# Kernel tuning notes

Measured on AMD Instinct MI355X. Metric: run time of the kernel, lower is better.

The kernel has to match this reference:

```python
import jax, jax.numpy as jnp
import numpy as np

EPS = 1e-5

def setup_inputs() -> dict:
    key = jax.random.key(0)
    ks = jax.random.split(key, 8)
    B, C, H, W = 8, 128, 128, 128
    return {
        "x1": jax.random.normal(ks[0], (B, C, H, W), jnp.float32),
        "x2": jax.random.normal(ks[1], (B, C, H, W), jnp.float32),
        "se_w1": jax.random.normal(ks[2], (C // 4, 2 * C), jnp.float32) * 0.05,
        "se_w2": jax.random.normal(ks[3], (2 * C, C // 4), jnp.float32) * 0.05,
        "conv_w": jax.random.normal(ks[4], (C, 2 * C, 3, 3), jnp.float32) * 0.05,
        "bn_gamma": jnp.ones((C,), jnp.float32),
        "bn_beta": jnp.zeros((C,), jnp.float32),
        "bn_mean": jax.random.normal(ks[5], (C,), jnp.float32) * 0.1,
        "bn_var": jax.random.uniform(ks[6], (C,), jnp.float32, 0.5, 1.5),
        "gamma": jax.random.uniform(ks[7], (1,), jnp.float32),
    }

def reference(x1, x2, se_w1, se_w2, conv_w, bn_gamma, bn_beta, bn_mean, bn_var, gamma):
    B, C, H, W = x1.shape
    x = jnp.concatenate([x1, x2], axis=1)                      # [B,2C,H,W]
    # SE gate: global avg pool -> Linear/ReLU/Linear/Sigmoid
    avg = jnp.mean(x, axis=(2, 3))                             # [B,2C]
    h = jax.nn.relu(avg @ se_w1.T)                             # [B,C//4]
    se = jax.nn.sigmoid(h @ se_w2.T)                           # [B,2C]
    x = x * se[:, :, None, None]
    # ConvBNReLU (3x3, pad 1, eval-mode BN)
    x = jax.lax.conv_general_dilated(
        x, conv_w, window_strides=(1, 1), padding="SAME",
        dimension_numbers=("NCHW", "OIHW", "NCHW"))           # [B,C,H,W]
    inv = bn_gamma / jnp.sqrt(bn_var + EPS)
    x = jax.nn.relu(x * inv[None, :, None, None]
                    + (bn_beta - bn_mean * inv)[None, :, None, None])
    # Channel self-attention with max-subtraction trick
    q = x.reshape(B, C, H * W)                                 # query = key = value
    sim = jnp.einsum("bcn,bdn->bcd", q, q)                     # [B,C,C]
    sim = jnp.max(sim, axis=-1, keepdims=True) - sim
    sim = jax.nn.softmax(sim, axis=-1)
    feat = jnp.einsum("bcd,bdn->bcn", sim, q).reshape(B, C, H, W)
    return gamma * feat + x
```

## Files before the change

kernel.cpp:

```cpp
#include <hip/hip_runtime.h>
#include <math.h>

#define B_   8
#define C_   128
#define C2_  256
#define H_   128
#define W_   128
#define HW_  16384
#define CR_  32
#define EPS_ 1e-5f
#define NS_  32

typedef _Float16 f16;
typedef f16 f16x8 __attribute__((ext_vector_type(8)));
typedef f16 f16x4 __attribute__((ext_vector_type(4)));
typedef float f32x4 __attribute__((ext_vector_type(4)));

__global__ __launch_bounds__(256) void prep_kernel(
    const float* __restrict__ x1, const float* __restrict__ x2,
    float* __restrict__ avg_sums, f16* __restrict__ xs)
{
    __shared__ f16 T[W_ * 136];
    __shared__ float part[C2_];
    int h = blockIdx.x, b = blockIdx.y;
    int tid = threadIdx.x;
    part[tid] = 0.f;
    f16* out = xs + ((size_t)b * H_ + h) * W_ * C2_;
    for (int p = 0; p < 2; ++p) {
        const float* src = p ? x2 : x1;
        __syncthreads();
        for (int idx = tid; idx < C_ * 32; idx += 256) {
            int c = idx >> 5, w4 = (idx & 31) << 2;
            const float4 v = *(const float4*)&src[(((size_t)b * C_ + c) * H_ + h) * W_ + w4];
            float s = v.x + v.y + v.z + v.w;
            s += __shfl_xor(s, 1, 64);  s += __shfl_xor(s, 2, 64);
            s += __shfl_xor(s, 4, 64);  s += __shfl_xor(s, 8, 64);
            s += __shfl_xor(s, 16, 64);
            if ((tid & 31) == 0) part[p * C_ + c] = s;
            int cs = c ^ (8 * ((idx & 31) & 15));
            T[(w4 + 0) * 136 + cs] = (f16)v.x;
            T[(w4 + 1) * 136 + cs] = (f16)v.y;
            T[(w4 + 2) * 136 + cs] = (f16)v.z;
            T[(w4 + 3) * 136 + cs] = (f16)v.w;
        }
        __syncthreads();
        for (int u = tid; u < W_ * 16; u += 256) {
            int w = u >> 4, o = u & 15;
            f16x8 v = *(const f16x8*)&T[w * 136 + ((o * 8) ^ (8 * ((w >> 2) & 15)))];
            *(f16x8*)&out[w * C2_ + p * C_ + o * 8] = v;
        }
    }
    __syncthreads();
    atomicAdd(&avg_sums[b * C2_ + tid], part[tid]);
}

__global__ __launch_bounds__(256) void se_mlp_kernel(
    const float* __restrict__ avg_sums, const float* __restrict__ w1,
    const float* __restrict__ w2, float* __restrict__ se)
{
    __shared__ float s_avg[B_ * C2_];
    __shared__ float s_h[B_ * CR_];
    for (int i = threadIdx.x; i < B_ * C2_; i += 256)
        s_avg[i] = avg_sums[i] * (1.f / (float)HW_);
    __syncthreads();
    {
        int i = threadIdx.x;
        int b = i / CR_, j = i % CR_;
        float s = 0.f;
        for (int k = 0; k < C2_; ++k) s += s_avg[b * C2_ + k] * w1[j * C2_ + k];
        s_h[i] = fmaxf(s, 0.f);
    }
    __syncthreads();
    for (int i = threadIdx.x; i < B_ * C2_; i += 256) {
        int b = i / C2_, c = i % C2_;
        float s = 0.f;
        #pragma unroll
        for (int j = 0; j < CR_; ++j) s += s_h[b * CR_ + j] * w2[c * CR_ + j];
        se[i] = 1.f / (1.f + expf(-s));
    }
}

__global__ __launch_bounds__(256) void wt_build_kernel(
    const float* __restrict__ conv_w, f16* __restrict__ wt)
{
    int idx = blockIdx.x * 256 + threadIdx.x;
    int ci = idx & 31;
    int co = (idx >> 5) & 127;
    int cc = (idx >> 12) & 7;
    int t  = idx >> 15;
    wt[idx] = (f16)conv_w[((size_t)co * C2_ + cc * 32 + ci) * 9 + t];
}

#define XROW 130
#define XPAD 40

__global__ __launch_bounds__(256, 3) void conv_mfma_kernel(
    const f16* __restrict__ xs, const f16* __restrict__ wt,
    const float* __restrict__ se,
    const float* __restrict__ bn_gamma, const float* __restrict__ bn_beta,
    const float* __restrict__ bn_mean, const float* __restrict__ bn_var,
    f16* __restrict__ yh, f16* __restrict__ yt)
{
    __shared__ f16 Xs[3 * XROW * XPAD];
    __shared__ __align__(16) f16 seh[C2_];
    int h = blockIdx.x, b = blockIdx.y;
    int tid = threadIdx.x;
    int wave = tid >> 6, lane = tid & 63;
    int wm = wave >> 1, wn = wave & 1;
    int lr = lane & 15, kg = lane >> 4;
    const f16* xsb = xs + (size_t)b * ((size_t)H_ * W_ * C2_);

    seh[tid] = (f16)se[b * C2_ + tid];

    f32x4 acc[4][4];
    #pragma unroll
    for (int i = 0; i < 4; ++i)
        #pragma unroll
        for (int j = 0; j < 4; ++j)
            #pragma unroll
            for (int r = 0; r < 4; ++r) acc[i][j][r] = 0.f;

    auto ldaf = [&](int cc, int t, f16x8* dst) {
        const f16* wb = wt + ((size_t)(t * 8 + cc) * C_) * 32;
        #pragma unroll
        for (int i = 0; i < 4; ++i)
            dst[i] = *(const f16x8*)&wb[(wm * 64 + i * 16 + lr) * 32 + kg * 8];
    };

    f16x8 af3[3][4];
    ldaf(0, 0, af3[0]);
    ldaf(0, 1, af3[1]);

    for (int cc = 0; cc < 8; ++cc) {
        __syncthreads();
        for (int u = tid; u < 3 * XROW * 4; u += 256) {
            int r = u / (XROW * 4);
            int rem = u - r * (XROW * 4);
            int col = rem >> 2, q = rem & 3;
            int gh = h + r - 1, gw = col - 1;
            f16x8 v;
            #pragma unroll
            for (int z = 0; z < 8; ++z) v[z] = (f16)0.f;
            if ((unsigned)gh < (unsigned)H_ && (unsigned)gw < (unsigned)W_) {
                v = *(const f16x8*)&xsb[((size_t)(gh * W_ + gw)) * C2_ + cc * 32 + q * 8];
                f16x8 sv = *(const f16x8*)&seh[cc * 32 + q * 8];
                v = v * sv;
            }
            *(f16x8*)&Xs[(r * XROW + col) * XPAD + q * 8] = v;
        }
        __syncthreads();
        #pragma unroll
        for (int t = 0; t < 9; ++t) {
            const int dh = t / 3, dw = t % 3;
            {
                int pt = t + 2, pcc = cc;
                if (pt >= 9) { pt -= 9; ++pcc; }
                if (pcc < 8) ldaf(pcc, pt, af3[(t + 2) % 3]);
            }
            f16x8 bf[4];
            #pragma unroll
            for (int j = 0; j < 4; ++j)
                bf[j] = *(const f16x8*)&Xs[(dh * XROW + (wn * 64 + j * 16 + lr + dw)) * XPAD + kg * 8];
            const f16x8* af = af3[t % 3];
            #pragma unroll
            for (int i = 0; i < 4; ++i)
                #pragma unroll
                for (int j = 0; j < 4; ++j)
                    acc[i][j] = __builtin_amdgcn_mfma_f32_16x16x32_f16(af[i], bf[j], acc[i][j], 0, 0, 0);
        }
    }
    #pragma unroll
    for (int i = 0; i < 4; ++i) {
        int cb = wm * 64 + i * 16 + kg * 4;
        float inv[4], add[4];
        #pragma unroll
        for (int r = 0; r < 4; ++r) {
            int c = cb + r;
            inv[r] = bn_gamma[c] * rsqrtf(bn_var[c] + EPS_);
            add[r] = bn_beta[c] - bn_mean[c] * inv[r];
        }
        #pragma unroll
        for (int j = 0; j < 4; ++j) {
            int n = wn * 64 + j * 16 + lr;
            f16x4 tv;
            #pragma unroll
            for (int r = 0; r < 4; ++r) {
                float v = fmaxf(acc[i][j][r] * inv[r] + add[r], 0.f);
                tv[r] = (f16)v;
                yh[((size_t)b * C_ + cb + r) * HW_ + h * W_ + n] = (f16)v;
            }
            *(f16x4*)&yt[((size_t)b * HW_ + h * W_ + n) * C_ + cb] = tv;
        }
    }
}

__global__ __launch_bounds__(512) void sim_mfma_kernel(
    const f16* __restrict__ yh, float* __restrict__ simp)
{
    int ns = blockIdx.x, b = blockIdx.y;
    int tid = threadIdx.x, wave = tid >> 6, lane = tid & 63;
    int wm = wave >> 2, wn = wave & 3;
    int lr = lane & 15, kg = lane >> 4;
    const f16* Y = yh + (size_t)b * C_ * HW_;
    int n0 = ns * (HW_ / NS_);

    f32x4 acc[4][2];
    #pragma unroll
    for (int i = 0; i < 4; ++i)
        #pragma unroll
        for (int j = 0; j < 2; ++j)
            #pragma unroll
            for (int r = 0; r < 4; ++r) acc[i][j][r] = 0.f;

    for (int kk = 0; kk < 16; ++kk) {
        int k = n0 + kk * 32 + kg * 8;
        f16x8 af[4], bf[2];
        #pragma unroll
        for (int i = 0; i < 4; ++i)
            af[i] = *(const f16x8*)&Y[(size_t)(wm * 64 + i * 16 + lr) * HW_ + k];
        #pragma unroll
        for (int j = 0; j < 2; ++j)
            bf[j] = *(const f16x8*)&Y[(size_t)(wn * 32 + j * 16 + lr) * HW_ + k];
        #pragma unroll
        for (int i = 0; i < 4; ++i)
            #pragma unroll
            for (int j = 0; j < 2; ++j)
                acc[i][j] = __builtin_amdgcn_mfma_f32_16x16x32_f16(af[i], bf[j], acc[i][j], 0, 0, 0);
    }
    float* dst = simp + (size_t)(ns * B_ + b) * C_ * C_;
    #pragma unroll
    for (int i = 0; i < 4; ++i)
        #pragma unroll
        for (int j = 0; j < 2; ++j)
            #pragma unroll
            for (int r = 0; r < 4; ++r)
                dst[(wm * 64 + i * 16 + kg * 4 + r) * C_ + wn * 32 + j * 16 + lr] = acc[i][j][r];
}

__global__ __launch_bounds__(128) void softmax_kernel(
    const float* __restrict__ simp, f16* __restrict__ Ph)
{
    int bc = blockIdx.x;
    int b = bc / C_;
    int d = threadIdx.x;
    float s = 0.f;
    for (int ns = 0; ns < NS_; ++ns)
        s += simp[((size_t)(ns * B_ + b) * C_ + (bc % C_)) * C_ + d];
    float v = -s;
    float m = v;
    #pragma unroll
    for (int off = 32; off > 0; off >>= 1) m = fmaxf(m, __shfl_xor(m, off, 64));
    __shared__ float sm[2], ss[2];
    int wid = threadIdx.x >> 6;
    if ((threadIdx.x & 63) == 0) sm[wid] = m;
    __syncthreads();
    m = fmaxf(sm[0], sm[1]);
    float p = expf(v - m);
    float sum = p;
    #pragma unroll
    for (int off = 32; off > 0; off >>= 1) sum += __shfl_xor(sum, off, 64);
    if ((threadIdx.x & 63) == 0) ss[wid] = sum;
    __syncthreads();
    sum = ss[0] + ss[1];
    Ph[(size_t)bc * C_ + d] = (f16)(p / sum);
}

__global__ __launch_bounds__(256) void feat_mfma_kernel(
    const f16* __restrict__ Ph, const f16* __restrict__ yt,
    const float* __restrict__ gamma, float* __restrict__ out)
{
    int nt = blockIdx.x, b = blockIdx.y;
    int tid = threadIdx.x, wave = tid >> 6, lane = tid & 63;
    int wm = wave >> 1, wn = wave & 1;
    int lr = lane & 15, kg = lane >> 4;
    int n0 = nt * 128;
    const f16* Pb = Ph + (size_t)b * C_ * C_;
    const f16* Yt = yt + (size_t)b * HW_ * C_;

    f32x4 acc[4][4];
    #pragma unroll
    for (int i = 0; i < 4; ++i)
        #pragma unroll
        for (int j = 0; j < 4; ++j)
            #pragma unroll
            for (int r = 0; r < 4; ++r) acc[i][j][r] = 0.f;

    #pragma unroll
    for (int kk = 0; kk < 4; ++kk) {
        int k = kk * 32 + kg * 8;
        f16x8 af[4], bf[4];
        #pragma unroll
        for (int i = 0; i < 4; ++i)
            af[i] = *(const f16x8*)&Pb[(wm * 64 + i * 16 + lr) * C_ + k];
        #pragma unroll
        for (int j = 0; j < 4; ++j)
            bf[j] = *(const f16x8*)&Yt[(size_t)(n0 + wn * 64 + j * 16 + lr) * C_ + k];
        #pragma unroll
        for (int i = 0; i < 4; ++i)
            #pragma unroll
            for (int j = 0; j < 4; ++j)
                acc[i][j] = __builtin_amdgcn_mfma_f32_16x16x32_f16(af[i], bf[j], acc[i][j], 0, 0, 0);
    }
    float g = gamma[0];
    #pragma unroll
    for (int i = 0; i < 4; ++i) {
        int cb = wm * 64 + i * 16 + kg * 4;
        #pragma unroll
        for (int j = 0; j < 4; ++j) {
            int n = n0 + wn * 64 + j * 16 + lr;
            f16x4 rv = *(const f16x4*)&Yt[(size_t)n * C_ + cb];
            #pragma unroll
            for (int r = 0; r < 4; ++r)
                out[((size_t)b * C_ + cb + r) * HW_ + n] = g * acc[i][j][r] + (float)rv[r];
        }
    }
}

extern "C" void kernel_launch(void* const* d_in, const int* in_sizes, int n_in,
                              void* d_out, int out_size, void* d_ws, size_t ws_size,
                              hipStream_t stream)
{
    const float* x1       = (const float*)d_in[0];
    const float* x2       = (const float*)d_in[1];
    const float* se_w1    = (const float*)d_in[2];
    const float* se_w2    = (const float*)d_in[3];
    const float* conv_w   = (const float*)d_in[4];
    const float* bn_gamma = (const float*)d_in[5];
    const float* bn_beta  = (const float*)d_in[6];
    const float* bn_mean  = (const float*)d_in[7];
    const float* bn_var   = (const float*)d_in[8];
    const float* gamma    = (const float*)d_in[9];
    float* out = (float*)d_out;

    char* ws = (char*)d_ws;
    float* avg  = (float*)(ws);
    float* se   = (float*)(ws + 8192);
    f16*   Ph   = (f16*)  (ws + 16384);
    f16*   wt   = (f16*)  (ws + 278528);
    f16*   xs   = (f16*)  (ws + 1048576);
    float* simp = (float*)(ws + 1048576);
    f16*   yh   = (f16*)  (ws + 68157440);
    f16*   yt   = (f16*)  (ws + 101711872);

    hipMemsetAsync(avg, 0, B_ * C2_ * sizeof(float), stream);
    prep_kernel<<<dim3(H_, B_), 256, 0, stream>>>(x1, x2, avg, xs);
    se_mlp_kernel<<<dim3(1), 256, 0, stream>>>(avg, se_w1, se_w2, se);
    wt_build_kernel<<<dim3(1152), 256, 0, stream>>>(conv_w, wt);
    conv_mfma_kernel<<<dim3(H_, B_), 256, 0, stream>>>(
        xs, wt, se, bn_gamma, bn_beta, bn_mean, bn_var, yh, yt);
    sim_mfma_kernel<<<dim3(NS_, B_), 512, 0, stream>>>(yh, simp);
    softmax_kernel<<<dim3(B_ * C_), 128, 0, stream>>>(simp, Ph);
    feat_mfma_kernel<<<dim3(HW_ / 128, B_), 256, 0, stream>>>(Ph, yt, gamma, out);
}
```

Measured before the change: 405.1 us.

## Compute two output rows per conv block and stage yt stores through LDS

The conv kernel now processes two output rows per block, with each wave covering all 128 output channels over 32 columns. Each weight fragment load is therefore reused across both rows, and the halo input tile is shared by four rows instead of three, with a new LDS layout indexed by channel group. The transposed yt output is written through shared memory so that global stores are coalesced 16-byte rows, and the feat kernel now reads the residual from the channel-major yh, so its residual reads match the output layout. In exchange, each thread holds more accumulators, occupancy drops to 2 blocks, the grid is halved, and the weight prefetch now only covers the next tap rather than two taps ahead.

```diff
diff --git a/kernel.cpp b/kernel.cpp
--- a/kernel.cpp
+++ b/kernel.cpp
@@ -91,53 +91,50 @@
     wt[idx] = (f16)conv_w[((size_t)co * C2_ + cc * 32 + ci) * 9 + t];
 }
 
-#define XROW 130
-#define XPAD 40
-
-__global__ __launch_bounds__(256, 3) void conv_mfma_kernel(
+__global__ __launch_bounds__(256, 2) void conv_mfma_kernel(
     const f16* __restrict__ xs, const f16* __restrict__ wt,
     const float* __restrict__ se,
     const float* __restrict__ bn_gamma, const float* __restrict__ bn_beta,
     const float* __restrict__ bn_mean, const float* __restrict__ bn_var,
     f16* __restrict__ yh, f16* __restrict__ yt)
 {
-    __shared__ f16 Xs[3 * XROW * XPAD];
+    __shared__ f16 Xs[17408];
     __shared__ __align__(16) f16 seh[C2_];
-    int h = blockIdx.x, b = blockIdx.y;
+    int h0 = blockIdx.x * 2, b = blockIdx.y;
     int tid = threadIdx.x;
     int wave = tid >> 6, lane = tid & 63;
-    int wm = wave >> 1, wn = wave & 1;
+    int wn = wave;
     int lr = lane & 15, kg = lane >> 4;
     const f16* xsb = xs + (size_t)b * ((size_t)H_ * W_ * C2_);
 
     seh[tid] = (f16)se[b * C2_ + tid];
 
-    f32x4 acc[4][4];
-    #pragma unroll
-    for (int i = 0; i < 4; ++i)
-        #pragma unroll
-        for (int j = 0; j < 4; ++j)
-            #pragma unroll
-            for (int r = 0; r < 4; ++r) acc[i][j][r] = 0.f;
-
+    f32x4 acc[2][8][2];
+    #pragma unroll
+    for (int o = 0; o < 2; ++o)
+        #pragma unroll
+        for (int i = 0; i < 8; ++i)
+            #pragma unroll
+            for (int j = 0; j < 2; ++j)
+                #pragma unroll
+                for (int r = 0; r < 4; ++r) acc[o][i][j][r] = 0.f;
+
+    f16x8 afb[2][8];
     auto ldaf = [&](int cc, int t, f16x8* dst) {
         const f16* wb = wt + ((size_t)(t * 8 + cc) * C_) * 32;
         #pragma unroll
-        for (int i = 0; i < 4; ++i)
-            dst[i] = *(const f16x8*)&wb[(wm * 64 + i * 16 + lr) * 32 + kg * 8];
+        for (int i = 0; i < 8; ++i)
+            dst[i] = *(const f16x8*)&wb[(i * 16 + lr) * 32 + kg * 8];
     };
 
-    f16x8 af3[3][4];
-    ldaf(0, 0, af3[0]);
-    ldaf(0, 1, af3[1]);
-
     for (int cc = 0; cc < 8; ++cc) {
         __syncthreads();
-        for (int u = tid; u < 3 * XROW * 4; u += 256) {
-            int r = u / (XROW * 4);
-            int rem = u - r * (XROW * 4);
+        ldaf(cc, 0, afb[0]);
+        for (int u = tid; u < 4 * 130 * 4; u += 256) {
+            int r = u / 520;
+            int rem = u - r * 520;
             int col = rem >> 2, q = rem & 3;
-            int gh = h + r - 1, gw = col - 1;
+            int gh = h0 - 1 + r, gw = col - 1;
             f16x8 v;
             #pragma unroll
             for (int z = 0; z < 8; ++z) v[z] = (f16)0.f;
@@ -146,50 +143,62 @@
                 f16x8 sv = *(const f16x8*)&seh[cc * 32 + q * 8];
                 v = v * sv;
             }
-            *(f16x8*)&Xs[(r * XROW + col) * XPAD + q * 8] = v;
+            *(f16x8*)&Xs[((r * 4 + q) * 132 + col) * 8] = v;
         }
         __syncthreads();
         #pragma unroll
         for (int t = 0; t < 9; ++t) {
             const int dh = t / 3, dw = t % 3;
-            {
-                int pt = t + 2, pcc = cc;
-                if (pt >= 9) { pt -= 9; ++pcc; }
-                if (pcc < 8) ldaf(pcc, pt, af3[(t + 2) % 3]);
-            }
-            f16x8 bf[4];
-            #pragma unroll
-            for (int j = 0; j < 4; ++j)
-                bf[j] = *(const f16x8*)&Xs[(dh * XROW + (wn * 64 + j * 16 + lr + dw)) * XPAD + kg * 8];
-            const f16x8* af = af3[t % 3];
-            #pragma unroll
-            for (int i = 0; i < 4; ++i)
+            if (t < 8) ldaf(cc, t + 1, afb[(t + 1) & 1]);
+            const f16x8* af = afb[t & 1];
+            #pragma unroll
+            for (int o = 0; o < 2; ++o) {
+                int r = o + dh;
+                f16x8 bf[2];
                 #pragma unroll
-                for (int j = 0; j < 4; ++j)
-                    acc[i][j] = __builtin_amdgcn_mfma_f32_16x16x32_f16(af[i], bf[j], acc[i][j], 0, 0, 0);
-        }
-    }
-    #pragma unroll
-    for (int i = 0; i < 4; ++i) {
-        int cb = wm * 64 + i * 16 + kg * 4;
-        float inv[4], add[4];
-        #pragma unroll
-        for (int r = 0; r < 4; ++r) {
-            int c = cb + r;
-            inv[r] = bn_gamma[c] * rsqrtf(bn_var[c] + EPS_);
-            add[r] = bn_beta[c] - bn_mean[c] * inv[r];
-        }
-        #pragma unroll
-        for (int j = 0; j < 4; ++j) {
-            int n = wn * 64 + j * 16 + lr;
-            f16x4 tv;
+                for (int j = 0; j < 2; ++j)
+                    bf[j] = *(const f16x8*)&Xs[((r * 4 + kg) * 132 +
+                                (wn * 32 + j * 16 + lr + dw)) * 8];
+                #pragma unroll
+                for (int i = 0; i < 8; ++i)
+                    #pragma unroll
+                    for (int j = 0; j < 2; ++j)
+                        acc[o][i][j] = __builtin_amdgcn_mfma_f32_16x16x32_f16(
+                            af[i], bf[j], acc[o][i][j], 0, 0, 0);
+            }
+        }
+    }
+    #pragma unroll
+    for (int o = 0; o < 2; ++o) {
+        __syncthreads();
+        #pragma unroll
+        for (int i = 0; i < 8; ++i) {
+            int cb = i * 16 + kg * 4;
+            float inv[4], add[4];
             #pragma unroll
             for (int r = 0; r < 4; ++r) {
-                float v = fmaxf(acc[i][j][r] * inv[r] + add[r], 0.f);
-                tv[r] = (f16)v;
-                yh[((size_t)b * C_ + cb + r) * HW_ + h * W_ + n] = (f16)v;
-            }
-            *(f16x4*)&yt[((size_t)b * HW_ + h * W_ + n) * C_ + cb] = tv;
+                int c = cb + r;
+                inv[r] = bn_gamma[c] * rsqrtf(bn_var[c] + EPS_);
+                add[r] = bn_beta[c] - bn_mean[c] * inv[r];
+            }
+            #pragma unroll
+            for (int j = 0; j < 2; ++j) {
+                int n = wn * 32 + j * 16 + lr;
+                f16x4 tv;
+                #pragma unroll
+                for (int r = 0; r < 4; ++r) {
+                    float v = fmaxf(acc[o][i][j][r] * inv[r] + add[r], 0.f);
+                    tv[r] = (f16)v;
+                    yh[((size_t)b * C_ + cb + r) * HW_ + (h0 + o) * W_ + n] = (f16)v;
+                }
+                *(f16x4*)&Xs[n * 136 + cb] = tv;
+            }
+        }
+        __syncthreads();
+        for (int u = tid; u < 128 * 16; u += 256) {
+            int n = u >> 4, o8 = u & 15;
+            f16x8 v = *(const f16x8*)&Xs[n * 136 + o8 * 8];
+            *(f16x8*)&yt[((size_t)b * HW_ + (h0 + o) * W_ + n) * C_ + o8 * 8] = v;
         }
     }
 }
@@ -267,6 +276,7 @@
 
 __global__ __launch_bounds__(256) void feat_mfma_kernel(
     const f16* __restrict__ Ph, const f16* __restrict__ yt,
+    const f16* __restrict__ yh,
     const float* __restrict__ gamma, float* __restrict__ out)
 {
     int nt = blockIdx.x, b = blockIdx.y;
@@ -308,10 +318,11 @@
         #pragma unroll
         for (int j = 0; j < 4; ++j) {
             int n = n0 + wn * 64 + j * 16 + lr;
-            f16x4 rv = *(const f16x4*)&Yt[(size_t)n * C_ + cb];
-            #pragma unroll
-            for (int r = 0; r < 4; ++r)
-                out[((size_t)b * C_ + cb + r) * HW_ + n] = g * acc[i][j][r] + (float)rv[r];
+            #pragma unroll
+            for (int r = 0; r < 4; ++r) {
+                float res = (float)yh[((size_t)b * C_ + cb + r) * HW_ + n];
+                out[((size_t)b * C_ + cb + r) * HW_ + n] = g * acc[i][j][r] + res;
+            }
         }
     }
 }
@@ -346,9 +357,9 @@
     prep_kernel<<<dim3(H_, B_), 256, 0, stream>>>(x1, x2, avg, xs);
     se_mlp_kernel<<<dim3(1), 256, 0, stream>>>(avg, se_w1, se_w2, se);
     wt_build_kernel<<<dim3(1152), 256, 0, stream>>>(conv_w, wt);
-    conv_mfma_kernel<<<dim3(H_, B_), 256, 0, stream>>>(
+    conv_mfma_kernel<<<dim3(H_ / 2, B_), 256, 0, stream>>>(
         xs, wt, se, bn_gamma, bn_beta, bn_mean, bn_var, yh, yt);
     sim_mfma_kernel<<<dim3(NS_, B_), 512, 0, stream>>>(yh, simp);
     softmax_kernel<<<dim3(B_ * C_), 128, 0, stream>>>(simp, Ph);
-    feat_mfma_kernel<<<dim3(HW_ / 128, B_), 256, 0, stream>>>(Ph, yt, gamma, out);
-}
+    feat_mfma_kernel<<<dim3(HW_ / 128, B_), 256, 0, stream>>>(Ph, yt, yh, gamma, out);
+}
```

New measurement: 389.0 us. 4.0% less time.
